# Kernel optimization log

Hardware: AMD Instinct MI355X
Metric: run time of the kernel (lower is better)

## Reference

```python
import jax, jax.numpy as jnp
import numpy as np


def _sum_of_sqrtm_factors(R1, R2):
    # QR of stacked square-root factors: returns upper-triangular R such that
    # R^T R = R1^T R1 + R2^T R2  (probdiffeq sqrtm.sum_of_sqrtm_factors)
    stacked = jnp.concatenate([R1, R2], axis=0)  # [2n, n]
    return jnp.linalg.qr(stacked, mode='reduced')[1]


def setup_inputs() -> dict:
    key = jax.random.key(0)
    k0, k1, k2, k3, k4 = jax.random.split(key, 5)
    n, d, T = 6, 1024, 4096  # n = num_derivatives + 1
    init_mean = jax.random.normal(k0, (n, d), dtype=jnp.float32)
    init_cov = jax.random.normal(k1, (n, n), dtype=jnp.float32) * 0.1
    # scale transitions so the T-step recursion stays numerically stable
    transitions = jax.random.normal(k2, (T, n, n), dtype=jnp.float32) * 0.2
    noise_means = jax.random.normal(k3, (T, n, d), dtype=jnp.float32)
    noise_covs = jax.random.normal(k4, (T, n, n), dtype=jnp.float32) * 0.1
    return {
        'init_mean': init_mean,
        'init_cov': init_cov,
        'transitions': transitions,
        'noise_means': noise_means,
        'noise_covs': noise_covs,
    }


def reference(init_mean, init_cov, transitions, noise_means, noise_covs):
    """IsotropicImplementation.marginalise_backwards: sequential Kalman
    smoother marginalisation via lax.scan of marginalise_model_isotropic."""

    def body(carry, x):
        m, l = carry                     # m: [n, d], l: [n, n]
        A, n_mean, n_l = x               # A: [n, n], n_mean: [n, d], n_l: [n, n]
        m_new = jnp.dot(A, m) + n_mean
        l_new = _sum_of_sqrtm_factors(jnp.dot(A, l).T, n_l.T).T
        out = (m_new, l_new)
        return out, out

    _, (means, covs) = jax.lax.scan(
        body, (init_mean, init_cov), (transitions, noise_means, noise_covs)
    )
    return means, covs  # [T, n, d], [T, n, n]
```

## Files before the change

kernel.cpp:

```cpp
#include <hip/hip_runtime.h>
#include <stdint.h>

#define T_STEPS 4096
#define DDIM    1024
#define CH      64
#define CL      64
#define MEAN_ELEMS ((size_t)T_STEPS * 6 * DDIM)

#define PF1 8
#define PF3 4

__device__ __forceinline__ float bf2f(uint16_t h){
    return __uint_as_float(((uint32_t)h) << 16);
}
__device__ __forceinline__ uint16_t f2bf(float f){
    uint32_t u = __float_as_uint(f);
    uint32_t r = 0x7FFFu + ((u >> 16) & 1u);
    return (uint16_t)((u + r) >> 16);
}
__device__ __forceinline__ float ld(const void* p, size_t idx, bool f32){
    return f32 ? ((const float*)p)[idx] : bf2f(((const uint16_t*)p)[idx]);
}
template<bool F32>
__device__ __forceinline__ float ldn(const void* p, size_t idx){
    return F32 ? ((const float*)p)[idx] : bf2f(((const uint16_t*)p)[idx]);
}

__global__ void k0_detect(const void* __restrict__ imean, uint32_t* __restrict__ flag){
    const uint32_t* w = (const uint32_t*)imean;
    int good = 0;
    for (int i = threadIdx.x; i < 3072; i += 64){
        float v = bf2f((uint16_t)(w[i] & 0xFFFFu));
        float a = fabsf(v);
        if (a > 1e-6f && a < 1e4f) good++;
    }
    #pragma unroll
    for (int ofs = 32; ofs >= 1; ofs >>= 1) good += __shfl_xor(good, ofs, 64);
    if (threadIdx.x == 0) flag[0] = (good < 2000) ? 1u : 0u;
}

__global__ void k1_chunk_compose(const void* __restrict__ trans,
                                 const void* __restrict__ ncov,
                                 double* __restrict__ Pd, double* __restrict__ Qd,
                                 float* __restrict__ Af, float* __restrict__ Pf,
                                 const uint32_t* __restrict__ flag){
    __shared__ float As[CL*36], Ns[CL*36];
    __shared__ double P_ds[36], Q_ds[36], T_ds[36];
    const bool f32 = flag[0] != 0;
    const int c = blockIdx.x;
    const int e = threadIdx.x;
    const int i = e / 6, j = e % 6;
    for (int idx = e; idx < CL*36; idx += 64){
        const size_t g = (size_t)c*CL*36 + idx;
        float a  = ld(trans, g, f32);
        float nn = ld(ncov,  g, f32);
        As[idx] = a; Ns[idx] = nn;
        Af[g] = a;
    }
    if (e < 36){ P_ds[e] = (i == j) ? 1.0 : 0.0; Q_ds[e] = 0.0; }
    __syncthreads();
    for (int s = 0; s < CL; ++s){
        double newP = 0.0, Tij = 0.0;
        if (e < 36){
            const float* A = As + s*36;
            #pragma unroll
            for (int m = 0; m < 6; ++m){
                double am = (double)A[i*6+m];
                newP += am * P_ds[m*6+j];
                Tij  += am * Q_ds[m*6+j];
            }
            T_ds[e] = Tij;
        }
        __syncthreads();
        if (e < 36){
            const float* A  = As + s*36;
            const float* Nn = Ns + s*36;
            double qn = 0.0;
            #pragma unroll
            for (int m = 0; m < 6; ++m){
                qn += T_ds[i*6+m] * (double)A[j*6+m];
                qn += (double)Nn[i*6+m] * (double)Nn[j*6+m];
            }
            P_ds[e] = newP;
            Q_ds[e] = qn;
        }
        __syncthreads();
    }
    if (e < 36){
        Pd[c*36+e] = P_ds[e];
        Qd[c*36+e] = Q_ds[e];
        Pf[c*36+e] = (float)P_ds[e];
    }
}

__global__ void k2_boundary_scan(const void* __restrict__ icov,
                                 const double* __restrict__ Pd,
                                 const double* __restrict__ Qd,
                                 double* __restrict__ Mb,
                                 const uint32_t* __restrict__ flag){
    __shared__ double Ps[CH][36], Qs[CH][36];
    __shared__ double M_ds[36], T_ds[36], l_ds[36];
    const bool f32 = flag[0] != 0;
    const int e = threadIdx.x;
    const int i = e / 6, j = e % 6;
    for (int idx = e; idx < CH*36; idx += 64){
        Ps[idx/36][idx%36] = Pd[idx];
        Qs[idx/36][idx%36] = Qd[idx];
    }
    if (e < 36) l_ds[e] = (double)ld(icov, e, f32);
    __syncthreads();
    if (e < 36){
        double m = 0.0;
        #pragma unroll
        for (int mm = 0; mm < 6; ++mm) m += l_ds[i*6+mm] * l_ds[j*6+mm];
        M_ds[e] = m; Mb[e] = m;
    }
    __syncthreads();
    for (int c = 0; c < CH - 1; ++c){
        if (e < 36){
            double t = 0.0;
            #pragma unroll
            for (int m = 0; m < 6; ++m) t += Ps[c][i*6+m] * M_ds[m*6+j];
            T_ds[e] = t;
        }
        __syncthreads();
        if (e < 36){
            double mn = 0.0;
            #pragma unroll
            for (int m = 0; m < 6; ++m) mn += T_ds[i*6+m] * Ps[c][j*6+m];
            mn += Qs[c][e];
            M_ds[e] = mn;
            Mb[(c+1)*36 + e] = mn;
        }
        __syncthreads();
    }
}

__global__ void k3_expand_M(const void* __restrict__ trans,
                            const void* __restrict__ ncov,
                            const double* __restrict__ Mb,
                            double* __restrict__ Mall,
                            const uint32_t* __restrict__ flag){
    __shared__ float As[CL*36], Ns[CL*36];
    __shared__ double M_ds[36], T_ds[36];
    const bool f32 = flag[0] != 0;
    const int c = blockIdx.x;
    const int e = threadIdx.x;
    const int i = e / 6, j = e % 6;
    for (int idx = e; idx < CL*36; idx += 64){
        const size_t g = (size_t)c*CL*36 + idx;
        As[idx] = ld(trans, g, f32);
        Ns[idx] = ld(ncov,  g, f32);
    }
    if (e < 36) M_ds[e] = Mb[c*36 + e];
    __syncthreads();
    for (int s = 0; s < CL; ++s){
        const int k = c * CL + s;
        if (e < 36) Mall[(size_t)k*36 + e] = M_ds[e];
        if (s == CL - 1) break;
        if (e < 36){
            const float* A = As + s*36;
            double t = 0.0;
            #pragma unroll
            for (int m = 0; m < 6; ++m) t += (double)A[i*6+m] * M_ds[m*6+j];
            T_ds[e] = t;
        }
        __syncthreads();
        if (e < 36){
            const float* A  = As + s*36;
            const float* Nn = Ns + s*36;
            double mn = 0.0;
            #pragma unroll
            for (int m = 0; m < 6; ++m){
                mn += T_ds[i*6+m] * (double)A[j*6+m];
                mn += (double)Nn[i*6+m] * (double)Nn[j*6+m];
            }
            M_ds[e] = mn;
        }
        __syncthreads();
    }
}

__global__ void __launch_bounds__(64)
k4_qr(const void* __restrict__ trans,
      const void* __restrict__ ncov,
      const void* __restrict__ icov,
      const double* __restrict__ Mall,
      void* __restrict__ d_out,
      uint32_t* __restrict__ masks,
      const uint32_t* __restrict__ flag){
    const int k = blockIdx.x * blockDim.x + threadIdx.x;
    if (k >= T_STEPS) return;
    const bool f32 = flag[0] != 0;
    double X[12][6];

    if (k == 0){
        double l0[6][6], A0[6][6];
        #pragma unroll
        for (int a = 0; a < 36; ++a){
            l0[a/6][a%6] = (double)ld(icov, a, f32);
            A0[a/6][a%6] = (double)ld(trans, a, f32);
        }
        #pragma unroll
        for (int i2 = 0; i2 < 6; ++i2)
            #pragma unroll
            for (int j2 = 0; j2 < 6; ++j2){
                double s = 0.0;
                #pragma unroll
                for (int m = 0; m < 6; ++m) s += A0[i2][m] * l0[m][j2];
                X[j2][i2] = s;
            }
    } else {
        double M[6][6];
        #pragma unroll
        for (int a = 0; a < 36; ++a) M[a/6][a%6] = Mall[(size_t)k*36 + a];
        #pragma unroll
        for (int j2 = 0; j2 < 6; ++j2){
            double d = M[j2][j2];
            #pragma unroll
            for (int m = 0; m < 6; ++m) if (m < j2) d -= M[j2][m]*M[j2][m];
            d = (d > 1e-300) ? d : 1e-300;
            double cjj = sqrt(d);
            M[j2][j2] = cjj;
            double inv = 1.0 / cjj;
            #pragma unroll
            for (int i2 = 0; i2 < 6; ++i2){
                if (i2 > j2){
                    double s = M[i2][j2];
                    #pragma unroll
                    for (int m = 0; m < 6; ++m) if (m < j2) s -= M[i2][m]*M[j2][m];
                    M[i2][j2] = s * inv;
                }
            }
        }
        #pragma unroll
        for (int i2 = 0; i2 < 6; ++i2){
            double Arow[6];
            #pragma unroll
            for (int m = 0; m < 6; ++m) Arow[m] = (double)ld(trans, (size_t)k*36 + i2*6 + m, f32);
            #pragma unroll
            for (int j2 = 0; j2 < 6; ++j2){
                double s = 0.0;
                #pragma unroll
                for (int m = 0; m < 6; ++m) if (m >= j2) s += Arow[m] * M[m][j2];
                X[j2][i2] = s;
            }
        }
    }
    #pragma unroll
    for (int r = 0; r < 6; ++r)
        #pragma unroll
        for (int c2 = 0; c2 < 6; ++c2)
            X[6+r][c2] = (double)ld(ncov, (size_t)k*36 + c2*6 + r, f32);

    #pragma unroll
    for (int kk = 0; kk < 6; ++kk){
        double alpha = X[kk][kk];
        double xn2 = 0.0;
        #pragma unroll
        for (int i2 = 0; i2 < 12; ++i2) if (i2 > kk) xn2 += X[i2][kk]*X[i2][kk];
        if (xn2 != 0.0){
            double nrm  = sqrt(alpha*alpha + xn2);
            double beta = (alpha >= 0.0) ? -nrm : nrm;
            double tau  = (beta - alpha) / beta;
            double sc   = 1.0 / (alpha - beta);
            #pragma unroll
            for (int i2 = 0; i2 < 12; ++i2) if (i2 > kk) X[i2][kk] *= sc;
            X[kk][kk] = beta;
            #pragma unroll
            for (int j2 = 0; j2 < 6; ++j2){
                if (j2 > kk){
                    double w = X[kk][j2];
                    #pragma unroll
                    for (int i2 = 0; i2 < 12; ++i2) if (i2 > kk) w += X[i2][kk]*X[i2][j2];
                    double wt = tau * w;
                    X[kk][j2] -= wt;
                    #pragma unroll
                    for (int i2 = 0; i2 < 12; ++i2) if (i2 > kk) X[i2][j2] -= X[i2][kk]*wt;
                }
            }
        }
    }

    uint32_t mask = 0;
    #pragma unroll
    for (int j2 = 0; j2 < 6; ++j2) if (X[j2][j2] < 0.0) mask |= (1u << j2);
    masks[k] = mask;

    if (f32){
        float* o = (float*)d_out + MEAN_ELEMS + (size_t)k*36;
        #pragma unroll
        for (int i2 = 0; i2 < 6; ++i2)
            #pragma unroll
            for (int j2 = 0; j2 < 6; ++j2)
                o[i2*6 + j2] = (j2 <= i2) ? (float)X[j2][i2] : 0.0f;
    } else {
        uint16_t* o = (uint16_t*)d_out + MEAN_ELEMS + (size_t)k*36;
        #pragma unroll
        for (int i2 = 0; i2 < 6; ++i2)
            #pragma unroll
            for (int j2 = 0; j2 < 6; ++j2)
                o[i2*6 + j2] = f2bf((j2 <= i2) ? (float)X[j2][i2] : 0.0f);
    }
}

__global__ void k5_scan(const uint32_t* __restrict__ masks, uint32_t* __restrict__ amask){
    const int lane = threadIdx.x;
    const int base = lane * 64;
    uint32_t tot = 0;
    for (int i2 = 0; i2 < 64; ++i2) tot ^= masks[base + i2];
    uint32_t incl = tot;
    #pragma unroll
    for (int ofs = 1; ofs < 64; ofs <<= 1){
        uint32_t up = (uint32_t)__shfl_up((int)incl, ofs, 64);
        if (lane >= ofs) incl ^= up;
    }
    uint32_t run = incl ^ tot;
    for (int i2 = 0; i2 < 64; ++i2){
        amask[base + i2] = run;
        run ^= masks[base + i2];
    }
}

__global__ void k6_apply(void* __restrict__ d_out, const uint32_t* __restrict__ amask,
                         const uint32_t* __restrict__ flag){
    const int k = blockIdx.x;
    const int e = threadIdx.x;
    if (k == 0 || e >= 36) return;
    const uint32_t m = amask[k];
    if (!((m >> (e % 6)) & 1u)) return;
    if (flag[0]) ((uint32_t*)d_out)[MEAN_ELEMS + (size_t)k*36 + e] ^= 0x80000000u;
    else         ((uint16_t*)d_out)[MEAN_ELEMS + (size_t)k*36 + e] ^= 0x8000u;
}

template<bool F32>
__device__ __forceinline__ void km1_body(const void* __restrict__ nmean,
                                         const float* __restrict__ As,
                                         float* __restrict__ r_ws, int c, int col){
    float r[6];
    #pragma unroll
    for (int i = 0; i < 6; ++i) r[i] = 0.f;
    float pb[PF1][6];
    const size_t base = (size_t)c*CL*6144 + col;
    #pragma unroll
    for (int p = 0; p < PF1; ++p)
        #pragma unroll
        for (int i = 0; i < 6; ++i)
            pb[p][i] = ldn<F32>(nmean, base + (size_t)p*6144 + i*DDIM);
    for (int s0 = 0; s0 < CL; s0 += PF1){
        const bool pf = (s0 + PF1 < CL);
        #pragma unroll
        for (int p = 0; p < PF1; ++p){
            const int s = s0 + p;
            float n[6];
            #pragma unroll
            for (int i = 0; i < 6; ++i) n[i] = pb[p][i];
            if (pf){
                #pragma unroll
                for (int i = 0; i < 6; ++i)
                    pb[p][i] = ldn<F32>(nmean, base + (size_t)(s + PF1)*6144 + i*DDIM);
            }
            const float* A = As + s*36;
            float acc[6];
            #pragma unroll
            for (int i = 0; i < 6; ++i){
                float t = n[i];
                #pragma unroll
                for (int m = 0; m < 6; ++m) t += A[i*6+m]*r[m];
                acc[i] = t;
            }
            #pragma unroll
            for (int i = 0; i < 6; ++i) r[i] = acc[i];
        }
    }
    float* out = r_ws + (size_t)c*6144;
    #pragma unroll
    for (int i = 0; i < 6; ++i) out[i*DDIM + col] = r[i];
}

__global__ void __launch_bounds__(256)
km1_chunk_r(const void* __restrict__ nmean, const float* __restrict__ Af,
            float* __restrict__ r_ws, const uint32_t* __restrict__ flag){
    __shared__ float As[CL*36];
    const int c = blockIdx.x >> 2;
    for (int idx = threadIdx.x; idx < CL*36; idx += 256)
        As[idx] = Af[(size_t)c*CL*36 + idx];
    __syncthreads();
    const int col = (blockIdx.x & 3)*256 + threadIdx.x;
    if (flag[0]) km1_body<true>(nmean, As, r_ws, c, col);
    else         km1_body<false>(nmean, As, r_ws, c, col);
}

__global__ void __launch_bounds__(256)
km2_scan(const void* __restrict__ imean,
         const float* __restrict__ Pf,
         const float* __restrict__ r_ws,
         float* __restrict__ mb_ws,
         const uint32_t* __restrict__ flag){
    __shared__ float Ps[CH*36];
    for (int idx = threadIdx.x; idx < CH*36; idx += 256) Ps[idx] = Pf[idx];
    __syncthreads();
    const bool f32 = flag[0] != 0;
    const int col = blockIdx.x*256 + threadIdx.x;
    float m[6];
    #pragma unroll
    for (int i = 0; i < 6; ++i) m[i] = ld(imean, (size_t)i*DDIM + col, f32);
    float rb[4][6];
    #pragma unroll
    for (int p = 0; p < 4; ++p)
        #pragma unroll
        for (int i = 0; i < 6; ++i) rb[p][i] = r_ws[(size_t)p*6144 + i*DDIM + col];
    for (int c0 = 0; c0 < CH; c0 += 4){
        const bool pf = (c0 + 4 < CH);
        #pragma unroll
        for (int p = 0; p < 4; ++p){
            const int c = c0 + p;
            float rc[6];
            #pragma unroll
            for (int i = 0; i < 6; ++i) rc[i] = rb[p][i];
            if (pf){
                #pragma unroll
                for (int i = 0; i < 6; ++i)
                    rb[p][i] = r_ws[(size_t)(c+4)*6144 + i*DDIM + col];
            }
            float* mb = mb_ws + (size_t)c*6144;
            #pragma unroll
            for (int i = 0; i < 6; ++i) mb[i*DDIM + col] = m[i];
            float nm[6];
            #pragma unroll
            for (int i = 0; i < 6; ++i){
                float s0 = rc[i];
                #pragma unroll
                for (int mm = 0; mm < 6; ++mm) s0 += Ps[c*36 + i*6+mm]*m[mm];
                nm[i] = s0;
            }
            #pragma unroll
            for (int i = 0; i < 6; ++i) m[i] = nm[i];
        }
    }
}

template<bool F32>
__device__ __forceinline__ void km3_body(const void* __restrict__ nmean,
                                         const float* __restrict__ As,
                                         const float* __restrict__ mb_ws,
                                         void* __restrict__ means_out,
                                         int c, int col){
    float m[6];
    const float* mb = mb_ws + (size_t)c*6144;
    #pragma unroll
    for (int i = 0; i < 6; ++i) m[i] = mb[i*DDIM + col];
    float pb[PF3][6];
    const size_t base = (size_t)c*CL*6144 + col;
    #pragma unroll
    for (int p = 0; p < PF3; ++p)
        #pragma unroll
        for (int i = 0; i < 6; ++i)
            pb[p][i] = ldn<F32>(nmean, base + (size_t)p*6144 + i*DDIM);
    for (int s0 = 0; s0 < CL; s0 += PF3){
        const bool pf = (s0 + PF3 < CL);
        #pragma unroll
        for (int p = 0; p < PF3; ++p){
            const int s = s0 + p;
            float n[6];
            #pragma unroll
            for (int i = 0; i < 6; ++i) n[i] = pb[p][i];
            if (pf){
                #pragma unroll
                for (int i = 0; i < 6; ++i)
                    pb[p][i] = ldn<F32>(nmean, base + (size_t)(s + PF3)*6144 + i*DDIM);
            }
            const int k = c*CL + s;
            const float* A = As + s*36;
            float acc[6];
            #pragma unroll
            for (int i = 0; i < 6; ++i){
                float t = n[i];
                #pragma unroll
                for (int mm = 0; mm < 6; ++mm) t += A[i*6+mm]*m[mm];
                acc[i] = t;
            }
            #pragma unroll
            for (int i = 0; i < 6; ++i){
                m[i] = acc[i];
                if (F32){
                    ((float*)means_out)[(size_t)k*6144 + i*DDIM + col] = m[i];
                } else {
                    ((uint16_t*)means_out)[(size_t)k*6144 + i*DDIM + col] = f2bf(m[i]);
                }
            }
        }
    }
}

__global__ void __launch_bounds__(256)
km3_final(const void* __restrict__ nmean, const float* __restrict__ Af,
          const float* __restrict__ mb_ws, void* __restrict__ means_out,
          const uint32_t* __restrict__ flag){
    __shared__ float As[CL*36];
    const int c = blockIdx.x >> 2;
    for (int idx = threadIdx.x; idx < CL*36; idx += 256)
        As[idx] = Af[(size_t)c*CL*36 + idx];
    __syncthreads();
    const int col = (blockIdx.x & 3)*256 + threadIdx.x;
    if (flag[0]) km3_body<true>(nmean, As, mb_ws, means_out, c, col);
    else         km3_body<false>(nmean, As, mb_ws, means_out, c, col);
}

extern "C" void kernel_launch(void* const* d_in, const int* in_sizes, int n_in,
                              void* d_out, int out_size, void* d_ws, size_t ws_size,
                              hipStream_t stream){
    (void)in_sizes; (void)n_in; (void)out_size; (void)ws_size;
    const void* imean = d_in[0];
    const void* icov  = d_in[1];
    const void* trans = d_in[2];
    const void* nmean = d_in[3];
    const void* ncov  = d_in[4];

    char* w = (char*)d_ws;
    double* Pd   = (double*)w; w += (size_t)CH*36*8;
    double* Qd   = (double*)w; w += (size_t)CH*36*8;
    double* Mb   = (double*)w; w += (size_t)CH*36*8;
    double* Mall = (double*)w; w += (size_t)T_STEPS*36*8;
    float*  Af   = (float*)w;  w += (size_t)T_STEPS*36*4;
    float*  Pf   = (float*)w;  w += (size_t)CH*36*4;
    uint32_t* masks = (uint32_t*)w; w += (size_t)T_STEPS*4;
    uint32_t* amask = (uint32_t*)w; w += (size_t)T_STEPS*4;
    uint32_t* flag  = (uint32_t*)w; w += 8;
    float* r_ws  = (float*)w;  w += (size_t)CH*6*DDIM*4;
    float* mb_ws = (float*)w;  w += (size_t)CH*6*DDIM*4;

    k0_detect<<<1, 64, 0, stream>>>(imean, flag);
    k1_chunk_compose<<<CH, 64, 0, stream>>>(trans, ncov, Pd, Qd, Af, Pf, flag);
    km1_chunk_r<<<4*CH, 256, 0, stream>>>(nmean, Af, r_ws, flag);
    km2_scan<<<4, 256, 0, stream>>>(imean, Pf, r_ws, mb_ws, flag);
    km3_final<<<4*CH, 256, 0, stream>>>(nmean, Af, mb_ws, d_out, flag);
    k2_boundary_scan<<<1, 64, 0, stream>>>(icov, Pd, Qd, Mb, flag);
    k3_expand_M<<<CH, 64, 0, stream>>>(trans, ncov, Mb, Mall, flag);
    k4_qr<<<T_STEPS/64, 64, 0, stream>>>(trans, ncov, icov, Mall, d_out, masks, flag);
    k5_scan<<<1, 64, 0, stream>>>(masks, amask);
    k6_apply<<<T_STEPS, 64, 0, stream>>>(d_out, amask, flag);
}
```

Before: 370.8 us.

## Fuse covariance expand with QR and sign scan with apply, inline dtype detection

Removes the standalone dtype-detect kernel by having every kernel recompute the flag redundantly from the first input. Merges M expansion with the per-step QR so the per-step covariances stay in shared memory rather than going through a global Mall buffer. Merges the sign-mask scan with the sign flip using per-chunk XOR totals. Also drops the Af copy of the transitions. Launch count falls from ten kernels to seven, at the price of repeated detection work in every block and QR running with only 64 blocks of 64 threads.

```diff
diff --git a/kernel.cpp b/kernel.cpp
--- a/kernel.cpp
+++ b/kernel.cpp
@@ -26,36 +26,41 @@
     return F32 ? ((const float*)p)[idx] : bf2f(((const uint16_t*)p)[idx]);
 }
 
-__global__ void k0_detect(const void* __restrict__ imean, uint32_t* __restrict__ flag){
+__device__ __forceinline__ uint32_t detect_wave(const void* imean){
     const uint32_t* w = (const uint32_t*)imean;
     int good = 0;
-    for (int i = threadIdx.x; i < 3072; i += 64){
+    for (int i = (int)(threadIdx.x & 63); i < 3072; i += 64){
         float v = bf2f((uint16_t)(w[i] & 0xFFFFu));
         float a = fabsf(v);
         if (a > 1e-6f && a < 1e4f) good++;
     }
     #pragma unroll
     for (int ofs = 32; ofs >= 1; ofs >>= 1) good += __shfl_xor(good, ofs, 64);
-    if (threadIdx.x == 0) flag[0] = (good < 2000) ? 1u : 0u;
-}
-
-__global__ void k1_chunk_compose(const void* __restrict__ trans,
-                                 const void* __restrict__ ncov,
-                                 double* __restrict__ Pd, double* __restrict__ Qd,
-                                 float* __restrict__ Af, float* __restrict__ Pf,
-                                 const uint32_t* __restrict__ flag){
+    return (good < 2000) ? 1u : 0u;
+}
+
+__global__ void __launch_bounds__(64)
+k1_chunk_compose(const void* __restrict__ imean,
+                 const void* __restrict__ trans,
+                 const void* __restrict__ ncov,
+                 double* __restrict__ Pd, double* __restrict__ Qd,
+                 float* __restrict__ Pf){
     __shared__ float As[CL*36], Ns[CL*36];
     __shared__ double P_ds[36], Q_ds[36], T_ds[36];
-    const bool f32 = flag[0] != 0;
+    __shared__ uint32_t s_flag;
     const int c = blockIdx.x;
     const int e = threadIdx.x;
     const int i = e / 6, j = e % 6;
+    {
+        uint32_t fl = detect_wave(imean);
+        if (e == 0) s_flag = fl;
+    }
+    __syncthreads();
+    const bool f32 = s_flag != 0;
     for (int idx = e; idx < CL*36; idx += 64){
         const size_t g = (size_t)c*CL*36 + idx;
-        float a  = ld(trans, g, f32);
-        float nn = ld(ncov,  g, f32);
-        As[idx] = a; Ns[idx] = nn;
-        Af[g] = a;
+        As[idx] = ld(trans, g, f32);
+        Ns[idx] = ld(ncov,  g, f32);
     }
     if (e < 36){ P_ds[e] = (i == j) ? 1.0 : 0.0; Q_ds[e] = 0.0; }
     __syncthreads();
@@ -93,16 +98,23 @@
     }
 }
 
-__global__ void k2_boundary_scan(const void* __restrict__ icov,
-                                 const double* __restrict__ Pd,
-                                 const double* __restrict__ Qd,
-                                 double* __restrict__ Mb,
-                                 const uint32_t* __restrict__ flag){
+__global__ void __launch_bounds__(64)
+k2_boundary_scan(const void* __restrict__ imean,
+                 const void* __restrict__ icov,
+                 const double* __restrict__ Pd,
+                 const double* __restrict__ Qd,
+                 double* __restrict__ Mb){
     __shared__ double Ps[CH][36], Qs[CH][36];
     __shared__ double M_ds[36], T_ds[36], l_ds[36];
-    const bool f32 = flag[0] != 0;
+    __shared__ uint32_t s_flag;
     const int e = threadIdx.x;
     const int i = e / 6, j = e % 6;
+    {
+        uint32_t fl = detect_wave(imean);
+        if (e == 0) s_flag = fl;
+    }
+    __syncthreads();
+    const bool f32 = s_flag != 0;
     for (int idx = e; idx < CH*36; idx += 64){
         Ps[idx/36][idx%36] = Pd[idx];
         Qs[idx/36][idx%36] = Qd[idx];
@@ -136,33 +148,43 @@
     }
 }
 
-__global__ void k3_expand_M(const void* __restrict__ trans,
-                            const void* __restrict__ ncov,
-                            const double* __restrict__ Mb,
-                            double* __restrict__ Mall,
-                            const uint32_t* __restrict__ flag){
+__global__ void __launch_bounds__(64)
+k34_expand_qr(const void* __restrict__ imean,
+              const void* __restrict__ icov,
+              const void* __restrict__ trans,
+              const void* __restrict__ ncov,
+              const double* __restrict__ Mb,
+              void* __restrict__ d_out,
+              uint32_t* __restrict__ masks,
+              uint32_t* __restrict__ chunkTot){
     __shared__ float As[CL*36], Ns[CL*36];
-    __shared__ double M_ds[36], T_ds[36];
-    const bool f32 = flag[0] != 0;
+    __shared__ double Mst[CL*37];
+    __shared__ double T_ds[36];
+    __shared__ uint32_t s_flag;
     const int c = blockIdx.x;
     const int e = threadIdx.x;
     const int i = e / 6, j = e % 6;
+    {
+        uint32_t fl = detect_wave(imean);
+        if (e == 0) s_flag = fl;
+    }
+    __syncthreads();
+    const bool f32 = s_flag != 0;
+
     for (int idx = e; idx < CL*36; idx += 64){
         const size_t g = (size_t)c*CL*36 + idx;
         As[idx] = ld(trans, g, f32);
         Ns[idx] = ld(ncov,  g, f32);
     }
-    if (e < 36) M_ds[e] = Mb[c*36 + e];
-    __syncthreads();
-    for (int s = 0; s < CL; ++s){
-        const int k = c * CL + s;
-        if (e < 36) Mall[(size_t)k*36 + e] = M_ds[e];
-        if (s == CL - 1) break;
+    if (e < 36) Mst[e] = Mb[c*36 + e];
+    __syncthreads();
+
+    for (int s = 0; s < CL - 1; ++s){
         if (e < 36){
             const float* A = As + s*36;
             double t = 0.0;
             #pragma unroll
-            for (int m = 0; m < 6; ++m) t += (double)A[i*6+m] * M_ds[m*6+j];
+            for (int m = 0; m < 6; ++m) t += (double)A[i*6+m] * Mst[s*37 + m*6+j];
             T_ds[e] = t;
         }
         __syncthreads();
@@ -175,31 +197,19 @@
                 mn += T_ds[i*6+m] * (double)A[j*6+m];
                 mn += (double)Nn[i*6+m] * (double)Nn[j*6+m];
             }
-            M_ds[e] = mn;
+            Mst[(s+1)*37 + e] = mn;
         }
         __syncthreads();
     }
-}
-
-__global__ void __launch_bounds__(64)
-k4_qr(const void* __restrict__ trans,
-      const void* __restrict__ ncov,
-      const void* __restrict__ icov,
-      const double* __restrict__ Mall,
-      void* __restrict__ d_out,
-      uint32_t* __restrict__ masks,
-      const uint32_t* __restrict__ flag){
-    const int k = blockIdx.x * blockDim.x + threadIdx.x;
-    if (k >= T_STEPS) return;
-    const bool f32 = flag[0] != 0;
+
+    const int k = c*CL + e;
     double X[12][6];
-
     if (k == 0){
         double l0[6][6], A0[6][6];
         #pragma unroll
         for (int a = 0; a < 36; ++a){
             l0[a/6][a%6] = (double)ld(icov, a, f32);
-            A0[a/6][a%6] = (double)ld(trans, a, f32);
+            A0[a/6][a%6] = (double)As[a];
         }
         #pragma unroll
         for (int i2 = 0; i2 < 6; ++i2)
@@ -213,7 +223,7 @@
     } else {
         double M[6][6];
         #pragma unroll
-        for (int a = 0; a < 36; ++a) M[a/6][a%6] = Mall[(size_t)k*36 + a];
+        for (int a = 0; a < 36; ++a) M[a/6][a%6] = Mst[e*37 + a];
         #pragma unroll
         for (int j2 = 0; j2 < 6; ++j2){
             double d = M[j2][j2];
@@ -237,7 +247,7 @@
         for (int i2 = 0; i2 < 6; ++i2){
             double Arow[6];
             #pragma unroll
-            for (int m = 0; m < 6; ++m) Arow[m] = (double)ld(trans, (size_t)k*36 + i2*6 + m, f32);
+            for (int m = 0; m < 6; ++m) Arow[m] = (double)As[e*36 + i2*6 + m];
             #pragma unroll
             for (int j2 = 0; j2 < 6; ++j2){
                 double s = 0.0;
@@ -251,7 +261,7 @@
     for (int r = 0; r < 6; ++r)
         #pragma unroll
         for (int c2 = 0; c2 < 6; ++c2)
-            X[6+r][c2] = (double)ld(ncov, (size_t)k*36 + c2*6 + r, f32);
+            X[6+r][c2] = (double)Ns[e*36 + c2*6 + r];
 
     #pragma unroll
     for (int kk = 0; kk < 6; ++kk){
@@ -287,6 +297,14 @@
     for (int j2 = 0; j2 < 6; ++j2) if (X[j2][j2] < 0.0) mask |= (1u << j2);
     masks[k] = mask;
 
+    uint32_t incl = mask;
+    #pragma unroll
+    for (int ofs = 1; ofs < 64; ofs <<= 1){
+        uint32_t up = (uint32_t)__shfl_up((int)incl, ofs, 64);
+        if (e >= ofs) incl ^= up;
+    }
+    if (e == 63) chunkTot[c] = incl;
+
     if (f32){
         float* o = (float*)d_out + MEAN_ELEMS + (size_t)k*36;
         #pragma unroll
@@ -304,33 +322,45 @@
     }
 }
 
-__global__ void k5_scan(const uint32_t* __restrict__ masks, uint32_t* __restrict__ amask){
-    const int lane = threadIdx.x;
-    const int base = lane * 64;
-    uint32_t tot = 0;
-    for (int i2 = 0; i2 < 64; ++i2) tot ^= masks[base + i2];
-    uint32_t incl = tot;
+__global__ void __launch_bounds__(64)
+k56_sign_apply(const void* __restrict__ imean,
+               void* __restrict__ d_out,
+               const uint32_t* __restrict__ masks,
+               const uint32_t* __restrict__ chunkTot){
+    __shared__ uint32_t s_flag;
+    const int c = blockIdx.x;
+    const int e = threadIdx.x;
+    {
+        uint32_t fl = detect_wave(imean);
+        if (e == 0) s_flag = fl;
+    }
+    __syncthreads();
+    const bool f32 = s_flag != 0;
+    const int k = c*CL + e;
+    const uint32_t m = masks[k];
+    uint32_t incl = m;
     #pragma unroll
     for (int ofs = 1; ofs < 64; ofs <<= 1){
         uint32_t up = (uint32_t)__shfl_up((int)incl, ofs, 64);
-        if (lane >= ofs) incl ^= up;
-    }
-    uint32_t run = incl ^ tot;
-    for (int i2 = 0; i2 < 64; ++i2){
-        amask[base + i2] = run;
-        run ^= masks[base + i2];
-    }
-}
-
-__global__ void k6_apply(void* __restrict__ d_out, const uint32_t* __restrict__ amask,
-                         const uint32_t* __restrict__ flag){
-    const int k = blockIdx.x;
-    const int e = threadIdx.x;
-    if (k == 0 || e >= 36) return;
-    const uint32_t m = amask[k];
-    if (!((m >> (e % 6)) & 1u)) return;
-    if (flag[0]) ((uint32_t*)d_out)[MEAN_ELEMS + (size_t)k*36 + e] ^= 0x80000000u;
-    else         ((uint16_t*)d_out)[MEAN_ELEMS + (size_t)k*36 + e] ^= 0x8000u;
+        if (e >= ofs) incl ^= up;
+    }
+    const uint32_t excl = incl ^ m;
+    uint32_t v = (e < c) ? chunkTot[e] : 0u;
+    #pragma unroll
+    for (int ofs = 32; ofs >= 1; ofs >>= 1) v ^= (uint32_t)__shfl_xor((int)v, ofs, 64);
+    const uint32_t am = v ^ excl;
+    if (am == 0u) return;
+    if (f32){
+        uint32_t* o = (uint32_t*)d_out + MEAN_ELEMS + (size_t)k*36;
+        #pragma unroll
+        for (int t = 0; t < 36; ++t)
+            if ((am >> (t % 6)) & 1u) o[t] ^= 0x80000000u;
+    } else {
+        uint16_t* o = (uint16_t*)d_out + MEAN_ELEMS + (size_t)k*36;
+        #pragma unroll
+        for (int t = 0; t < 36; ++t)
+            if ((am >> (t % 6)) & 1u) o[t] ^= 0x8000u;
+    }
 }
 
 template<bool F32>
@@ -379,28 +409,41 @@
 }
 
 __global__ void __launch_bounds__(256)
-km1_chunk_r(const void* __restrict__ nmean, const float* __restrict__ Af,
-            float* __restrict__ r_ws, const uint32_t* __restrict__ flag){
+km1_chunk_r(const void* __restrict__ imean, const void* __restrict__ trans,
+            const void* __restrict__ nmean,
+            float* __restrict__ r_ws){
     __shared__ float As[CL*36];
+    __shared__ uint32_t s_flag;
+    if (threadIdx.x < 64){
+        uint32_t fl = detect_wave(imean);
+        if (threadIdx.x == 0) s_flag = fl;
+    }
+    __syncthreads();
+    const bool f32 = s_flag != 0;
     const int c = blockIdx.x >> 2;
     for (int idx = threadIdx.x; idx < CL*36; idx += 256)
-        As[idx] = Af[(size_t)c*CL*36 + idx];
+        As[idx] = ld(trans, (size_t)c*CL*36 + idx, f32);
     __syncthreads();
     const int col = (blockIdx.x & 3)*256 + threadIdx.x;
-    if (flag[0]) km1_body<true>(nmean, As, r_ws, c, col);
-    else         km1_body<false>(nmean, As, r_ws, c, col);
+    if (f32) km1_body<true >(nmean, As, r_ws, c, col);
+    else     km1_body<false>(nmean, As, r_ws, c, col);
 }
 
 __global__ void __launch_bounds__(256)
 km2_scan(const void* __restrict__ imean,
          const float* __restrict__ Pf,
          const float* __restrict__ r_ws,
-         float* __restrict__ mb_ws,
-         const uint32_t* __restrict__ flag){
+         float* __restrict__ mb_ws){
     __shared__ float Ps[CH*36];
+    __shared__ uint32_t s_flag;
+    if (threadIdx.x < 64){
+        uint32_t fl = detect_wave(imean);
+        if (threadIdx.x == 0) s_flag = fl;
+    }
+    __syncthreads();
+    const bool f32 = s_flag != 0;
     for (int idx = threadIdx.x; idx < CH*36; idx += 256) Ps[idx] = Pf[idx];
     __syncthreads();
-    const bool f32 = flag[0] != 0;
     const int col = blockIdx.x*256 + threadIdx.x;
     float m[6];
     #pragma unroll
@@ -494,17 +537,24 @@
 }
 
 __global__ void __launch_bounds__(256)
-km3_final(const void* __restrict__ nmean, const float* __restrict__ Af,
-          const float* __restrict__ mb_ws, void* __restrict__ means_out,
-          const uint32_t* __restrict__ flag){
+km3_final(const void* __restrict__ imean, const void* __restrict__ trans,
+          const void* __restrict__ nmean,
+          const float* __restrict__ mb_ws, void* __restrict__ means_out){
     __shared__ float As[CL*36];
+    __shared__ uint32_t s_flag;
+    if (threadIdx.x < 64){
+        uint32_t fl = detect_wave(imean);
+        if (threadIdx.x == 0) s_flag = fl;
+    }
+    __syncthreads();
+    const bool f32 = s_flag != 0;
     const int c = blockIdx.x >> 2;
     for (int idx = threadIdx.x; idx < CL*36; idx += 256)
-        As[idx] = Af[(size_t)c*CL*36 + idx];
+        As[idx] = ld(trans, (size_t)c*CL*36 + idx, f32);
     __syncthreads();
     const int col = (blockIdx.x & 3)*256 + threadIdx.x;
-    if (flag[0]) km3_body<true>(nmean, As, mb_ws, means_out, c, col);
-    else         km3_body<false>(nmean, As, mb_ws, means_out, c, col);
+    if (f32) km3_body<true >(nmean, As, mb_ws, means_out, c, col);
+    else     km3_body<false>(nmean, As, mb_ws, means_out, c, col);
 }
 
 extern "C" void kernel_launch(void* const* d_in, const int* in_sizes, int n_in,
@@ -521,23 +571,17 @@
     double* Pd   = (double*)w; w += (size_t)CH*36*8;
     double* Qd   = (double*)w; w += (size_t)CH*36*8;
     double* Mb   = (double*)w; w += (size_t)CH*36*8;
-    double* Mall = (double*)w; w += (size_t)T_STEPS*36*8;
-    float*  Af   = (float*)w;  w += (size_t)T_STEPS*36*4;
     float*  Pf   = (float*)w;  w += (size_t)CH*36*4;
-    uint32_t* masks = (uint32_t*)w; w += (size_t)T_STEPS*4;
-    uint32_t* amask = (uint32_t*)w; w += (size_t)T_STEPS*4;
-    uint32_t* flag  = (uint32_t*)w; w += 8;
+    uint32_t* masks    = (uint32_t*)w; w += (size_t)T_STEPS*4;
+    uint32_t* chunkTot = (uint32_t*)w; w += (size_t)CH*4;
     float* r_ws  = (float*)w;  w += (size_t)CH*6*DDIM*4;
     float* mb_ws = (float*)w;  w += (size_t)CH*6*DDIM*4;
 
-    k0_detect<<<1, 64, 0, stream>>>(imean, flag);
-    k1_chunk_compose<<<CH, 64, 0, stream>>>(trans, ncov, Pd, Qd, Af, Pf, flag);
-    km1_chunk_r<<<4*CH, 256, 0, stream>>>(nmean, Af, r_ws, flag);
-    km2_scan<<<4, 256, 0, stream>>>(imean, Pf, r_ws, mb_ws, flag);
-    km3_final<<<4*CH, 256, 0, stream>>>(nmean, Af, mb_ws, d_out, flag);
-    k2_boundary_scan<<<1, 64, 0, stream>>>(icov, Pd, Qd, Mb, flag);
-    k3_expand_M<<<CH, 64, 0, stream>>>(trans, ncov, Mb, Mall, flag);
-    k4_qr<<<T_STEPS/64, 64, 0, stream>>>(trans, ncov, icov, Mall, d_out, masks, flag);
-    k5_scan<<<1, 64, 0, stream>>>(masks, amask);
-    k6_apply<<<T_STEPS, 64, 0, stream>>>(d_out, amask, flag);
-}
+    k1_chunk_compose<<<CH, 64, 0, stream>>>(imean, trans, ncov, Pd, Qd, Pf);
+    k2_boundary_scan<<<1, 64, 0, stream>>>(imean, icov, Pd, Qd, Mb);
+    km1_chunk_r<<<4*CH, 256, 0, stream>>>(imean, trans, nmean, r_ws);
+    km2_scan<<<4, 256, 0, stream>>>(imean, Pf, r_ws, mb_ws);
+    km3_final<<<4*CH, 256, 0, stream>>>(imean, trans, nmean, mb_ws, d_out);
+    k34_expand_qr<<<CH, 64, 0, stream>>>(imean, icov, trans, ncov, Mb, d_out, masks, chunkTot);
+    k56_sign_apply<<<CH, 64, 0, stream>>>(imean, d_out, masks, chunkTot);
+}
```

Result: no change. 375.4 us (+1.2%).
